# Performance work log

Measured on AMD Instinct MI355X. Metric: run time of the kernel, lower is better.

Reference implementation:

```python
import jax, jax.numpy as jnp
import numpy as np

EPS = 1e-8


def _similarity(feat):
    # feat: [b, c, h, w] -> pixel-pair cosine-similarity matrix [b, hw, hw]
    b, c, h, w = feat.shape
    feat = feat.astype(jnp.float32)
    # channel-wise L2 norm per pixel, eps added AFTER sqrt (matches torch code)
    norm = jnp.sqrt(jnp.sum(feat * feat, axis=1, keepdims=True)) + EPS  # [b,1,h,w]
    f = (feat / norm).reshape(b, c, h * w)                              # [b,c,hw]
    return jnp.einsum('icm,icn->imn', f, f)                             # [b,hw,hw]


def _sim_distance(feat1, feat2):
    b, _, h, w = feat1.shape
    hw = h * w
    sim_err = (_similarity(feat1) - _similarity(feat2)) ** 2 / (hw * hw) / b
    return jnp.sum(sim_err)


def setup_inputs() -> dict:
    key = jax.random.key(0)
    k1, k2, k3, k4 = jax.random.split(key, 4)
    return {
        'res1_t': jax.random.normal(k1, (4, 128, 64, 64), dtype=jnp.float32),
        'res1_s': jax.random.normal(k2, (4, 128, 64, 64), dtype=jnp.float32),
        'res2_t': jax.random.normal(k3, (4, 256, 32, 32), dtype=jnp.float32),
        'res2_s': jax.random.normal(k4, (4, 256, 32, 32), dtype=jnp.float32),
    }


def reference(res1_t, res1_s, res2_t, res2_s):
    # teacher features are detached in the original; forward math is identical
    pwl_g1 = _sim_distance(res1_t, res1_s)
    pwl_g2 = _sim_distance(res2_t, res2_s)
    loss = pwl_g1 + pwl_g2
    return (loss, jnp.stack([loss, pwl_g1, pwl_g2]))
```

## Files before the change

### kernel.cpp

```cpp
#include <hip/hip_runtime.h>
#include <math.h>

#define EPSF 1e-8f

typedef __attribute__((ext_vector_type(4))) short short4v;
typedef __attribute__((ext_vector_type(8))) short short8v;
typedef __attribute__((ext_vector_type(4))) float float4v;

__device__ inline short f2bf(float f) {
    unsigned u = __builtin_bit_cast(unsigned, f);
    unsigned r = (u + 0x7FFFu + ((u >> 16) & 1u)) >> 16;
    return (short)r;
}
__device__ inline float bf2f(short s) {
    unsigned u = ((unsigned)(unsigned short)s) << 16;
    return __builtin_bit_cast(float, u);
}

#define F1T 0
#define F1S 2097152
#define F2T 4194304
#define F2S 5242880

__constant__ int g1_tab[10][4] = {
    {0,0,0,1},{0,0,1,2},{0,1,1,1},
    {1,0,0,1},{1,0,1,2},{1,1,1,1},
    {2,0,0,-2},{2,0,1,-2},{2,1,0,-2},{2,1,1,-2},
};
__constant__ int g2_tab[36][4] = {
    {0,0,0,1},{0,0,1,2},{0,0,2,2},{0,0,3,2},{0,1,1,1},{0,1,2,2},{0,1,3,2},{0,2,2,1},{0,2,3,2},{0,3,3,1},
    {1,0,0,1},{1,0,1,2},{1,0,2,2},{1,0,3,2},{1,1,1,1},{1,1,2,2},{1,1,3,2},{1,2,2,1},{1,2,3,2},{1,3,3,1},
    {2,0,0,-2},{2,0,1,-2},{2,0,2,-2},{2,0,3,-2},
    {2,1,0,-2},{2,1,1,-2},{2,1,2,-2},{2,1,3,-2},
    {2,2,0,-2},{2,2,1,-2},{2,2,2,-2},{2,2,3,-2},
    {2,3,0,-2},{2,3,1,-2},{2,3,2,-2},{2,3,3,-2},
};

template<int C, int HW>
__device__ inline void prep_body(const float* __restrict__ x,
                                 short* __restrict__ f, int lp, int t)
{
    const int lanei = t & 7, slice = t >> 3;
    const int b = lp / HW, m = lp - b * HW;
    const float* p = x + (size_t)b * C * HW + m;
    short*       q = f + (size_t)b * C * HW + m;
    constexpr int CPR = C >> 5;
    short4v vals[CPR];
    float4 s0 = {0.f,0.f,0.f,0.f}, s1 = {0.f,0.f,0.f,0.f};
#pragma unroll
    for (int i = 0; i < CPR; i += 2) {
        float4 v0 = *(const float4*)(p + (size_t)(slice * CPR + i)     * HW);
        float4 v1 = *(const float4*)(p + (size_t)(slice * CPR + i + 1) * HW);
        s0.x += v0.x * v0.x; s0.y += v0.y * v0.y;
        s0.z += v0.z * v0.z; s0.w += v0.w * v0.w;
        s1.x += v1.x * v1.x; s1.y += v1.y * v1.y;
        s1.z += v1.z * v1.z; s1.w += v1.w * v1.w;
        vals[i]     = (short4v){ f2bf(v0.x), f2bf(v0.y), f2bf(v0.z), f2bf(v0.w) };
        vals[i + 1] = (short4v){ f2bf(v1.x), f2bf(v1.y), f2bf(v1.z), f2bf(v1.w) };
    }
    float4 s = { s0.x + s1.x, s0.y + s1.y, s0.z + s1.z, s0.w + s1.w };
    __shared__ float4 red[32][8];
    __shared__ float4 invl[8];
    red[slice][lanei] = s;
    __syncthreads();
    if (t < 8) {
        float4 tot = {0.f,0.f,0.f,0.f};
#pragma unroll
        for (int sl = 0; sl < 32; ++sl) {
            float4 v = red[sl][t];
            tot.x += v.x; tot.y += v.y; tot.z += v.z; tot.w += v.w;
        }
        invl[t] = (float4){ 1.f / (sqrtf(tot.x) + EPSF), 1.f / (sqrtf(tot.y) + EPSF),
                            1.f / (sqrtf(tot.z) + EPSF), 1.f / (sqrtf(tot.w) + EPSF) };
    }
    __syncthreads();
    const float4 iv = invl[lanei];
#pragma unroll
    for (int i = 0; i < CPR; ++i) {
        const int r = slice * CPR + i;
        short4v rv = vals[i];
        short4v o = { f2bf(bf2f(rv[0]) * iv.x), f2bf(bf2f(rv[1]) * iv.y),
                      f2bf(bf2f(rv[2]) * iv.z), f2bf(bf2f(rv[3]) * iv.w) };
        *(short4v*)(q + (size_t)r * HW) = o;
    }
}

__global__ __launch_bounds__(256) void prep_kernel(
    const float* __restrict__ x1t, const float* __restrict__ x1s,
    const float* __restrict__ x2t, const float* __restrict__ x2s,
    short* __restrict__ F, float* __restrict__ out,
    unsigned* __restrict__ counter)
{
    const int gp = blockIdx.x * 32;
    const int t = threadIdx.x;
    const int lanei = t & 7;
    if (blockIdx.x == 0 && t < 4) out[t] = 0.f;
    if (blockIdx.x == 0 && t == 4) *counter = 0u;
    if (gp < 16384)
        prep_body<128, 4096>(x1t, F + F1T, gp + lanei * 4, t);
    else if (gp < 32768)
        prep_body<128, 4096>(x1s, F + F1S, gp - 16384 + lanei * 4, t);
    else if (gp < 36864)
        prep_body<256, 1024>(x2t, F + F2T, gp - 32768 + lanei * 4, t);
    else
        prep_body<256, 1024>(x2s, F + F2S, gp - 36864 + lanei * 4, t);
}

#define LSTR 136

template<int HW, bool SHARE>
__device__ inline void gram_tile(const short* __restrict__ Fa,
                                 const short* __restrict__ Fb,
                                 int k0, int t,
                                 short* __restrict__ ldsA,
                                 short* __restrict__ ldsB,
                                 float4v (&acc)[2][2])
{
    const int lane = t & 63, w = t >> 6;
    const int r16 = lane & 15, quad = lane >> 4;
    const int srow = t >> 4, skc = t & 15;
    const int rt2 = (w >> 1) * 2, ct2 = (w & 1) * 2;

    short8v ar[4], br[4];
#pragma unroll
    for (int p = 0; p < 4; ++p)
        ar[p] = *(const short8v*)(Fa + (size_t)(p * 16 + srow) * HW + k0 + skc * 8);
    if (!SHARE) {
#pragma unroll
        for (int p = 0; p < 4; ++p)
            br[p] = *(const short8v*)(Fb + (size_t)(p * 16 + srow) * HW + k0 + skc * 8);
    }

#pragma unroll 1
    for (int st = 0; st < 4; ++st) {
#pragma unroll
        for (int p = 0; p < 4; ++p)
            *(short8v*)(ldsA + (p * 16 + srow) * LSTR + skc * 8) = ar[p];
        if (!SHARE) {
#pragma unroll
            for (int p = 0; p < 4; ++p)
                *(short8v*)(ldsB + (p * 16 + srow) * LSTR + skc * 8) = br[p];
        }
        __syncthreads();
        if (st < 3) {
            const int k1 = k0 + (st + 1) * 128;
#pragma unroll
            for (int p = 0; p < 4; ++p)
                ar[p] = *(const short8v*)(Fa + (size_t)(p * 16 + srow) * HW + k1 + skc * 8);
            if (!SHARE) {
#pragma unroll
                for (int p = 0; p < 4; ++p)
                    br[p] = *(const short8v*)(Fb + (size_t)(p * 16 + srow) * HW + k1 + skc * 8);
            }
        }
        const short* A = ldsA;
        const short* B = SHARE ? ldsA : ldsB;
#pragma unroll
        for (int ks = 0; ks < 4; ++ks) {
            short8v af[2], bf[2];
#pragma unroll
            for (int i = 0; i < 2; ++i)
                af[i] = *(const short8v*)(A + ((rt2 + i) * 16 + r16) * LSTR + ks * 32 + quad * 8);
#pragma unroll
            for (int j = 0; j < 2; ++j)
                bf[j] = *(const short8v*)(B + ((ct2 + j) * 16 + r16) * LSTR + ks * 32 + quad * 8);
#pragma unroll
            for (int i = 0; i < 2; ++i)
#pragma unroll
                for (int j = 0; j < 2; ++j)
                    acc[i][j] = __builtin_amdgcn_mfma_f32_16x16x32_bf16(
                        af[i], bf[j], acc[i][j], 0, 0, 0);
        }
        __syncthreads();
    }
}

__global__ __launch_bounds__(256, 4) void gramA_kernel(
    const short* __restrict__ F, float* __restrict__ partials)
{
    __shared__ __align__(16) short ldsA[64 * LSTR];
    __shared__ __align__(16) short ldsB[64 * LSTR];

    const int id = blockIdx.x;
    const int t = threadIdx.x, w = t >> 6, lane = t & 63;
    const int r16 = lane & 15, quad = lane >> 4;

    float4v acc[2][2];
#pragma unroll
    for (int i = 0; i < 2; ++i)
#pragma unroll
        for (int j = 0; j < 2; ++j) acc[i][j] = (float4v){0.f, 0.f, 0.f, 0.f};

    if (id < 320) {
        const int comb = id >> 5, sub = id & 31;
        const int b = sub >> 3, ks = sub & 7;
        const int g = g1_tab[comb][0];
        const int ra = g1_tab[comb][1] << 6, rb = g1_tab[comb][2] << 6;
        const short* Fa = (g == 1 ? F + F1S : F + F1T) + (size_t)(b * 128 + ra) * 4096;
        const short* Fb = (g == 0 ? F + F1T : F + F1S) + (size_t)(b * 128 + rb) * 4096;
        const int k0 = ks * 512;
        if (g < 2 && ra == rb) gram_tile<4096, true >(Fa, Fa, k0, t, ldsA, ldsB, acc);
        else                   gram_tile<4096, false>(Fa, Fb, k0, t, ldsA, ldsB, acc);
    } else {
        const int id2 = id - 320;
        const int comb = id2 >> 3, sub = id2 & 7;
        const int b = sub >> 1, ks = sub & 1;
        const int g = g2_tab[comb][0];
        const int ra = g2_tab[comb][1] << 6, rb = g2_tab[comb][2] << 6;
        const short* Fa = (g == 1 ? F + F2S : F + F2T) + (size_t)(b * 256 + ra) * 1024;
        const short* Fb = (g == 0 ? F + F2T : F + F2S) + (size_t)(b * 256 + rb) * 1024;
        const int k0 = ks * 512;
        if (g < 2 && ra == rb) gram_tile<1024, true >(Fa, Fa, k0, t, ldsA, ldsB, acc);
        else                   gram_tile<1024, false>(Fa, Fb, k0, t, ldsA, ldsB, acc);
    }

    float* dst = partials + (size_t)id * 4096;
    const int rt2 = (w >> 1) * 2, ct2 = (w & 1) * 2;
#pragma unroll
    for (int i = 0; i < 2; ++i)
#pragma unroll
        for (int j = 0; j < 2; ++j)
#pragma unroll
            for (int r = 0; r < 4; ++r)
                dst[((rt2 + i) * 16 + quad * 4 + r) * 64 + (ct2 + j) * 16 + r16]
                    = acc[i][j][r];
}

__global__ __launch_bounds__(1024) void gramB_kernel(
    const float* __restrict__ partials, float* __restrict__ out,
    unsigned* __restrict__ counter)
{
    __shared__ float scratch[16];
    const int tile = blockIdx.x;
    const int t = threadIdx.x, lane = t & 63, w = t >> 6;

    const float* base; int P; float wt; int which;
    if (tile < 40) {
        const int comb = tile >> 2, b = tile & 3;
        base = partials + (size_t)(comb * 32 + b * 8) * 4096;
        P = 8;
        wt = (float)g1_tab[comb][3] * (1.0f / (4096.f * 4096.f * 4.f));
        which = 2;
    } else {
        const int t2 = tile - 40;
        const int comb = t2 >> 2, b = t2 & 3;
        base = partials + (size_t)(320 + comb * 8 + b * 2) * 4096;
        P = 2;
        wt = (float)g2_tab[comb][3] * (1.0f / (1024.f * 1024.f * 4.f));
        which = 3;
    }

    const int off = t * 4;
    float4 v = {0.f, 0.f, 0.f, 0.f};
    if (P == 8) {
#pragma unroll
        for (int p = 0; p < 8; ++p) {
            float4 u = *(const float4*)(base + (size_t)p * 4096 + off);
            v.x += u.x; v.y += u.y; v.z += u.z; v.w += u.w;
        }
    } else {
#pragma unroll
        for (int p = 0; p < 2; ++p) {
            float4 u = *(const float4*)(base + (size_t)p * 4096 + off);
            v.x += u.x; v.y += u.y; v.z += u.z; v.w += u.w;
        }
    }
    float s = (v.x * v.x + v.y * v.y + v.z * v.z + v.w * v.w) * wt;

#pragma unroll
    for (int o = 32; o > 0; o >>= 1) s += __shfl_down(s, o);
    if (lane == 0) scratch[w] = s;
    __syncthreads();
    if (t == 0) {
        float val = 0.f;
#pragma unroll
        for (int i = 0; i < 16; ++i) val += scratch[i];
        atomicAdd(&out[which], val);
        __threadfence();
        unsigned old = atomicAdd(counter, 1u);
        if (old == 183u) {
            float g1v = __hip_atomic_load(&out[2], __ATOMIC_RELAXED,
                                          __HIP_MEMORY_SCOPE_AGENT);
            float g2v = __hip_atomic_load(&out[3], __ATOMIC_RELAXED,
                                          __HIP_MEMORY_SCOPE_AGENT);
            float loss = g1v + g2v;
            out[0] = loss;
            out[1] = loss;
        }
    }
}

extern "C" void kernel_launch(void* const* d_in, const int* in_sizes, int n_in,
                              void* d_out, int out_size, void* d_ws, size_t ws_size,
                              hipStream_t stream)
{
    const float* x1t = (const float*)d_in[0];
    const float* x1s = (const float*)d_in[1];
    const float* x2t = (const float*)d_in[2];
    const float* x2s = (const float*)d_in[3];

    short* F         = (short*)d_ws;
    float* partials  = (float*)d_ws + 3200000;
    unsigned* counter = (unsigned*)((float*)d_ws + 5700000);

    prep_kernel<<<1280, 256, 0, stream>>>(x1t, x1s, x2t, x2s, F,
                                          (float*)d_out, counter);
    gramA_kernel<<<608, 256, 0, stream>>>(F, partials);
    gramB_kernel<<<184, 1024, 0, stream>>>(partials, (float*)d_out, counter);
}
```

Baseline: 93.63 us.

## Use 128x128 Gram tiles and fuse partial reduction via last-block counters

```diff
diff --git a/kernel.cpp b/kernel.cpp
--- a/kernel.cpp
+++ b/kernel.cpp
@@ -22,18 +22,10 @@
 #define F2T 4194304
 #define F2S 5242880
 
-__constant__ int g1_tab[10][4] = {
+__constant__ int g2q_tab[10][4] = {
     {0,0,0,1},{0,0,1,2},{0,1,1,1},
     {1,0,0,1},{1,0,1,2},{1,1,1,1},
     {2,0,0,-2},{2,0,1,-2},{2,1,0,-2},{2,1,1,-2},
-};
-__constant__ int g2_tab[36][4] = {
-    {0,0,0,1},{0,0,1,2},{0,0,2,2},{0,0,3,2},{0,1,1,1},{0,1,2,2},{0,1,3,2},{0,2,2,1},{0,2,3,2},{0,3,3,1},
-    {1,0,0,1},{1,0,1,2},{1,0,2,2},{1,0,3,2},{1,1,1,1},{1,1,2,2},{1,1,3,2},{1,2,2,1},{1,2,3,2},{1,3,3,1},
-    {2,0,0,-2},{2,0,1,-2},{2,0,2,-2},{2,0,3,-2},
-    {2,1,0,-2},{2,1,1,-2},{2,1,2,-2},{2,1,3,-2},
-    {2,2,0,-2},{2,2,1,-2},{2,2,2,-2},{2,2,3,-2},
-    {2,3,0,-2},{2,3,1,-2},{2,3,2,-2},{2,3,3,-2},
 };
 
 template<int C, int HW>
@@ -89,13 +81,13 @@
     const float* __restrict__ x1t, const float* __restrict__ x1s,
     const float* __restrict__ x2t, const float* __restrict__ x2s,
     short* __restrict__ F, float* __restrict__ out,
-    unsigned* __restrict__ counter)
+    unsigned* __restrict__ cnt)
 {
     const int gp = blockIdx.x * 32;
     const int t = threadIdx.x;
     const int lanei = t & 7;
     if (blockIdx.x == 0 && t < 4) out[t] = 0.f;
-    if (blockIdx.x == 0 && t == 4) *counter = 0u;
+    if (blockIdx.x == 0 && t >= 8 && t < 61) cnt[t - 8] = 0u;
     if (gp < 16384)
         prep_body<128, 4096>(x1t, F + F1T, gp + lanei * 4, t);
     else if (gp < 32768)
@@ -106,68 +98,68 @@
         prep_body<256, 1024>(x2s, F + F2S, gp - 36864 + lanei * 4, t);
 }
 
-#define LSTR 136
+#define ASTR 72
 
 template<int HW, bool SHARE>
-__device__ inline void gram_tile(const short* __restrict__ Fa,
-                                 const short* __restrict__ Fb,
-                                 int k0, int t,
-                                 short* __restrict__ ldsA,
-                                 short* __restrict__ ldsB,
-                                 float4v (&acc)[2][2])
+__device__ inline void gram_tile128(const short* __restrict__ Fa,
+                                    const short* __restrict__ Fb,
+                                    int k0, int t,
+                                    short* __restrict__ ldsA,
+                                    short* __restrict__ ldsB,
+                                    float4v (&acc)[4][4])
 {
     const int lane = t & 63, w = t >> 6;
     const int r16 = lane & 15, quad = lane >> 4;
-    const int srow = t >> 4, skc = t & 15;
-    const int rt2 = (w >> 1) * 2, ct2 = (w & 1) * 2;
+    const int wr = w >> 1, wc = w & 1;
+    const int srow = t >> 3, skc = (t & 7) * 8;
 
     short8v ar[4], br[4];
 #pragma unroll
     for (int p = 0; p < 4; ++p)
-        ar[p] = *(const short8v*)(Fa + (size_t)(p * 16 + srow) * HW + k0 + skc * 8);
+        ar[p] = *(const short8v*)(Fa + (size_t)(p * 32 + srow) * HW + k0 + skc);
     if (!SHARE) {
 #pragma unroll
         for (int p = 0; p < 4; ++p)
-            br[p] = *(const short8v*)(Fb + (size_t)(p * 16 + srow) * HW + k0 + skc * 8);
+            br[p] = *(const short8v*)(Fb + (size_t)(p * 32 + srow) * HW + k0 + skc);
     }
 
 #pragma unroll 1
-    for (int st = 0; st < 4; ++st) {
+    for (int st = 0; st < 8; ++st) {
 #pragma unroll
         for (int p = 0; p < 4; ++p)
-            *(short8v*)(ldsA + (p * 16 + srow) * LSTR + skc * 8) = ar[p];
+            *(short8v*)(ldsA + (p * 32 + srow) * ASTR + skc) = ar[p];
         if (!SHARE) {
 #pragma unroll
             for (int p = 0; p < 4; ++p)
-                *(short8v*)(ldsB + (p * 16 + srow) * LSTR + skc * 8) = br[p];
+                *(short8v*)(ldsB + (p * 32 + srow) * ASTR + skc) = br[p];
         }
         __syncthreads();
-        if (st < 3) {
-            const int k1 = k0 + (st + 1) * 128;
+        if (st < 7) {
+            const int k1 = k0 + (st + 1) * 64;
 #pragma unroll
             for (int p = 0; p < 4; ++p)
-                ar[p] = *(const short8v*)(Fa + (size_t)(p * 16 + srow) * HW + k1 + skc * 8);
+                ar[p] = *(const short8v*)(Fa + (size_t)(p * 32 + srow) * HW + k1 + skc);
             if (!SHARE) {
 #pragma unroll
                 for (int p = 0; p < 4; ++p)
-                    br[p] = *(const short8v*)(Fb + (size_t)(p * 16 + srow) * HW + k1 + skc * 8);
+                    br[p] = *(const short8v*)(Fb + (size_t)(p * 32 + srow) * HW + k1 + skc);
             }
         }
         const short* A = ldsA;
         const short* B = SHARE ? ldsA : ldsB;
 #pragma unroll
-        for (int ks = 0; ks < 4; ++ks) {
-            short8v af[2], bf[2];
-#pragma unroll
-            for (int i = 0; i < 2; ++i)
-                af[i] = *(const short8v*)(A + ((rt2 + i) * 16 + r16) * LSTR + ks * 32 + quad * 8);
-#pragma unroll
-            for (int j = 0; j < 2; ++j)
-                bf[j] = *(const short8v*)(B + ((ct2 + j) * 16 + r16) * LSTR + ks * 32 + quad * 8);
-#pragma unroll
-            for (int i = 0; i < 2; ++i)
-#pragma unroll
-                for (int j = 0; j < 2; ++j)
+        for (int ks = 0; ks < 2; ++ks) {
+            short8v af[4], bf[4];
+#pragma unroll
+            for (int i = 0; i < 4; ++i)
+                af[i] = *(const short8v*)(A + (wr * 64 + i * 16 + r16) * ASTR + ks * 32 + quad * 8);
+#pragma unroll
+            for (int j = 0; j < 4; ++j)
+                bf[j] = *(const short8v*)(B + (wc * 64 + j * 16 + r16) * ASTR + ks * 32 + quad * 8);
+#pragma unroll
+            for (int i = 0; i < 4; ++i)
+#pragma unroll
+                for (int j = 0; j < 4; ++j)
                     acc[i][j] = __builtin_amdgcn_mfma_f32_16x16x32_bf16(
                         af[i], bf[j], acc[i][j], 0, 0, 0);
         }
@@ -175,117 +167,109 @@
     }
 }
 
-__global__ __launch_bounds__(256, 4) void gramA_kernel(
-    const short* __restrict__ F, float* __restrict__ partials)
-{
-    __shared__ __align__(16) short ldsA[64 * LSTR];
-    __shared__ __align__(16) short ldsB[64 * LSTR];
+__global__ __launch_bounds__(256, 2) void gram_kernel(
+    const short* __restrict__ F, float* __restrict__ partials,
+    float* __restrict__ out, unsigned* __restrict__ cnt)
+{
+    __shared__ __align__(16) short ldsA[128 * ASTR];
+    __shared__ __align__(16) short ldsB[128 * ASTR];
+    __shared__ float sc[4];
+    __shared__ int fin;
 
     const int id = blockIdx.x;
     const int t = threadIdx.x, w = t >> 6, lane = t & 63;
     const int r16 = lane & 15, quad = lane >> 4;
-
-    float4v acc[2][2];
-#pragma unroll
-    for (int i = 0; i < 2; ++i)
-#pragma unroll
-        for (int j = 0; j < 2; ++j) acc[i][j] = (float4v){0.f, 0.f, 0.f, 0.f};
-
-    if (id < 320) {
-        const int comb = id >> 5, sub = id & 31;
-        const int b = sub >> 3, ks = sub & 7;
-        const int g = g1_tab[comb][0];
-        const int ra = g1_tab[comb][1] << 6, rb = g1_tab[comb][2] << 6;
-        const short* Fa = (g == 1 ? F + F1S : F + F1T) + (size_t)(b * 128 + ra) * 4096;
-        const short* Fb = (g == 0 ? F + F1T : F + F1S) + (size_t)(b * 128 + rb) * 4096;
+    const int wr = w >> 1, wc = w & 1;
+
+    float4v acc[4][4];
+#pragma unroll
+    for (int i = 0; i < 4; ++i)
+#pragma unroll
+        for (int j = 0; j < 4; ++j) acc[i][j] = (float4v){0.f, 0.f, 0.f, 0.f};
+
+    int tile, P, slab, slab0, which;
+    float wt;
+    if (id < 96) {
+        const int jb = id >> 3, ks = id & 7;
+        const int type = jb >> 2, b = jb & 3;
         const int k0 = ks * 512;
-        if (g < 2 && ra == rb) gram_tile<4096, true >(Fa, Fa, k0, t, ldsA, ldsB, acc);
-        else                   gram_tile<4096, false>(Fa, Fb, k0, t, ldsA, ldsB, acc);
-    } else {
-        const int id2 = id - 320;
-        const int comb = id2 >> 3, sub = id2 & 7;
-        const int b = sub >> 1, ks = sub & 1;
-        const int g = g2_tab[comb][0];
-        const int ra = g2_tab[comb][1] << 6, rb = g2_tab[comb][2] << 6;
-        const short* Fa = (g == 1 ? F + F2S : F + F2T) + (size_t)(b * 256 + ra) * 1024;
-        const short* Fb = (g == 0 ? F + F2T : F + F2S) + (size_t)(b * 256 + rb) * 1024;
-        const int k0 = ks * 512;
-        if (g < 2 && ra == rb) gram_tile<1024, true >(Fa, Fa, k0, t, ldsA, ldsB, acc);
-        else                   gram_tile<1024, false>(Fa, Fb, k0, t, ldsA, ldsB, acc);
-    }
-
-    float* dst = partials + (size_t)id * 4096;
-    const int rt2 = (w >> 1) * 2, ct2 = (w & 1) * 2;
-#pragma unroll
-    for (int i = 0; i < 2; ++i)
-#pragma unroll
-        for (int j = 0; j < 2; ++j)
-#pragma unroll
-            for (int r = 0; r < 4; ++r)
-                dst[((rt2 + i) * 16 + quad * 4 + r) * 64 + (ct2 + j) * 16 + r16]
-                    = acc[i][j][r];
-}
-
-__global__ __launch_bounds__(1024) void gramB_kernel(
-    const float* __restrict__ partials, float* __restrict__ out,
-    unsigned* __restrict__ counter)
-{
-    __shared__ float scratch[16];
-    const int tile = blockIdx.x;
-    const int t = threadIdx.x, lane = t & 63, w = t >> 6;
-
-    const float* base; int P; float wt; int which;
-    if (tile < 40) {
-        const int comb = tile >> 2, b = tile & 3;
-        base = partials + (size_t)(comb * 32 + b * 8) * 4096;
-        P = 8;
-        wt = (float)g1_tab[comb][3] * (1.0f / (4096.f * 4096.f * 4.f));
+        const short* Fa = (type == 1 ? F + F1S : F + F1T) + (size_t)b * 524288;
+        const short* Fb = (type == 0 ? F + F1T : F + F1S) + (size_t)b * 524288;
+        if (type < 2) gram_tile128<4096, true >(Fa, Fa, k0, t, ldsA, ldsB, acc);
+        else          gram_tile128<4096, false>(Fa, Fb, k0, t, ldsA, ldsB, acc);
+        tile = jb; P = 8; slab0 = jb * 8; slab = slab0 + ks;
+        wt = (type == 2 ? -2.f : 1.f) * (1.0f / (4096.f * 4096.f * 4.f));
         which = 2;
     } else {
-        const int t2 = tile - 40;
-        const int comb = t2 >> 2, b = t2 & 3;
-        base = partials + (size_t)(320 + comb * 8 + b * 2) * 4096;
-        P = 2;
-        wt = (float)g2_tab[comb][3] * (1.0f / (1024.f * 1024.f * 4.f));
+        const int id2 = id - 96;
+        const int job = id2 >> 1, ks = id2 & 1;
+        const int b = job / 10, j10 = job - b * 10;
+        const int type = g2q_tab[j10][0];
+        const int qi = g2q_tab[j10][1], qj = g2q_tab[j10][2];
+        const int k0 = ks * 512;
+        const short* Fa = (type == 1 ? F + F2S : F + F2T)
+                          + (size_t)(b * 256 + qi * 128) * 1024;
+        const short* Fb = (type == 0 ? F + F2T : F + F2S)
+                          + (size_t)(b * 256 + qj * 128) * 1024;
+        if (type < 2 && qi == qj)
+            gram_tile128<1024, true >(Fa, Fa, k0, t, ldsA, ldsB, acc);
+        else
+            gram_tile128<1024, false>(Fa, Fb, k0, t, ldsA, ldsB, acc);
+        tile = 12 + job; P = 2; slab0 = 96 + job * 2; slab = slab0 + ks;
+        wt = (float)g2q_tab[j10][3] * (1.0f / (1024.f * 1024.f * 4.f));
         which = 3;
     }
 
-    const int off = t * 4;
-    float4 v = {0.f, 0.f, 0.f, 0.f};
-    if (P == 8) {
-#pragma unroll
-        for (int p = 0; p < 8; ++p) {
-            float4 u = *(const float4*)(base + (size_t)p * 4096 + off);
-            v.x += u.x; v.y += u.y; v.z += u.z; v.w += u.w;
-        }
-    } else {
-#pragma unroll
-        for (int p = 0; p < 2; ++p) {
-            float4 u = *(const float4*)(base + (size_t)p * 4096 + off);
-            v.x += u.x; v.y += u.y; v.z += u.z; v.w += u.w;
-        }
-    }
-    float s = (v.x * v.x + v.y * v.y + v.z * v.z + v.w * v.w) * wt;
-
-#pragma unroll
-    for (int o = 32; o > 0; o >>= 1) s += __shfl_down(s, o);
-    if (lane == 0) scratch[w] = s;
+    float* dst = partials + (size_t)slab * 16384;
+#pragma unroll
+    for (int i = 0; i < 4; ++i)
+#pragma unroll
+        for (int j = 0; j < 4; ++j)
+#pragma unroll
+            for (int r = 0; r < 4; ++r)
+                dst[(wr * 64 + i * 16 + quad * 4 + r) * 128 + wc * 64 + j * 16 + r16]
+                    = acc[i][j][r];
+
     __syncthreads();
     if (t == 0) {
-        float val = 0.f;
-#pragma unroll
-        for (int i = 0; i < 16; ++i) val += scratch[i];
-        atomicAdd(&out[which], val);
         __threadfence();
-        unsigned old = atomicAdd(counter, 1u);
-        if (old == 183u) {
-            float g1v = __hip_atomic_load(&out[2], __ATOMIC_RELAXED,
-                                          __HIP_MEMORY_SCOPE_AGENT);
-            float g2v = __hip_atomic_load(&out[3], __ATOMIC_RELAXED,
-                                          __HIP_MEMORY_SCOPE_AGENT);
-            float loss = g1v + g2v;
-            out[0] = loss;
-            out[1] = loss;
+        unsigned old = atomicAdd(&cnt[tile], 1u);
+        fin = (old == (unsigned)(P - 1)) ? 1 : 0;
+    }
+    __syncthreads();
+    if (fin) {
+        __threadfence();
+        const float* base = partials + (size_t)slab0 * 16384;
+        float s = 0.f;
+#pragma unroll 1
+        for (int c = 0; c < 16; ++c) {
+            const int idx = (c * 256 + t) * 4;
+            float4 v = {0.f, 0.f, 0.f, 0.f};
+            for (int p = 0; p < P; ++p) {
+                float4 u = *(const float4*)(base + (size_t)p * 16384 + idx);
+                v.x += u.x; v.y += u.y; v.z += u.z; v.w += u.w;
+            }
+            s += v.x * v.x + v.y * v.y + v.z * v.z + v.w * v.w;
+        }
+        s *= wt;
+#pragma unroll
+        for (int o = 32; o > 0; o >>= 1) s += __shfl_down(s, o);
+        if (lane == 0) sc[w] = s;
+        __syncthreads();
+        if (t == 0) {
+            float val = sc[0] + sc[1] + sc[2] + sc[3];
+            atomicAdd(&out[which], val);
+            __threadfence();
+            unsigned gold = atomicAdd(&cnt[52], 1u);
+            if (gold == 51u) {
+                float g1v = __hip_atomic_load(&out[2], __ATOMIC_RELAXED,
+                                              __HIP_MEMORY_SCOPE_AGENT);
+                float g2v = __hip_atomic_load(&out[3], __ATOMIC_RELAXED,
+                                              __HIP_MEMORY_SCOPE_AGENT);
+                float loss = g1v + g2v;
+                out[0] = loss;
+                out[1] = loss;
+            }
         }
     }
 }
@@ -301,10 +285,9 @@
 
     short* F         = (short*)d_ws;
     float* partials  = (float*)d_ws + 3200000;
-    unsigned* counter = (unsigned*)((float*)d_ws + 5700000);
+    unsigned* cnt    = (unsigned*)((float*)d_ws + 6200000);
 
     prep_kernel<<<1280, 256, 0, stream>>>(x1t, x1s, x2t, x2s, F,
-                                          (float*)d_out, counter);
-    gramA_kernel<<<608, 256, 0, stream>>>(F, partials);
-    gramB_kernel<<<184, 1024, 0, stream>>>(partials, (float*)d_out, counter);
-}
+                                          (float*)d_out, cnt);
+    gram_kernel<<<176, 256, 0, stream>>>(F, partials, (float*)d_out, cnt);
+}
```

Result: slower. 139.8 us (+49.3%).
